# Optimization experiments

Measured on AMD Instinct MI355X. Metric: run time of the kernel, lower is better.

## Reference

```python
import jax, jax.numpy as jnp
import numpy as np

NC = 6            # CPAB tessellation cells (tess_size=6, zero_boundary=True)
DIM = NC - 1      # theta dimension = 5
SIG_LEN = 2048
CHANNELS = 3
BATCH = 256
FC_IN = 64 * 168  # flattened net_part1 output for signal_len=2048
NUM_SCALING = 0   # N in transform_data_ss
EPS_BN = 1e-5


def _cpab_basis():
    """QR null-space basis of the CPAB continuity + zero-boundary constraints.
    Params ordered [a_1,b_1,...,a_NC,b_NC]; v(x)=a_c x + b_c on cell c."""
    nc = NC
    L = np.zeros((nc + 1, 2 * nc))
    for k in range(1, nc):  # continuity at internal knots x_k = k/nc
        xk = k / nc
        L[k - 1, 2 * (k - 1)] = xk
        L[k - 1, 2 * (k - 1) + 1] = 1.0
        L[k - 1, 2 * k] = -xk
        L[k - 1, 2 * k + 1] = -1.0
    L[nc - 1, 1] = 1.0        # v(0) = 0  -> b_1 = 0
    L[nc, 2 * (nc - 1)] = 1.0  # v(1) = 0 -> a_nc + b_nc = 0
    L[nc, 2 * nc - 1] = 1.0
    Q, _ = np.linalg.qr(L.T, mode='complete')
    return np.ascontiguousarray(Q[:, nc + 1:]).astype(np.float32)  # (12, 5)


def _conv1d(x, w, b):
    y = jax.lax.conv_general_dilated(x, w, (1,), 'VALID',
                                     dimension_numbers=('NCH', 'OIH', 'NCH'))
    return y + b[None, :, None]


def _maxpool1d(x, k, s):
    return jax.lax.reduce_window(x, -jnp.inf, jax.lax.max, (1, 1, k), (1, 1, s), 'VALID')


def _bn(x, g, b, m, v):  # eval-mode BatchNorm1d
    return (x - m[None, :, None]) * (g / jnp.sqrt(v + EPS_BN))[None, :, None] + b[None, :, None]


def _integrate(x, A):
    """Exact CPAB 1D flow integration over t=1 with cell-crossing handling.
    x: (B, n) points in [0,1]; A: (B, NC, 2) per-cell (a, b). Monotone
    trajectories cross at most NC-1 boundaries -> fixed NC+1 iterations."""
    a_all, b_all = A[:, :, 0], A[:, :, 1]
    t = jnp.ones_like(x)
    for _ in range(NC + 1):
        c = jnp.clip(jnp.floor(x * NC).astype(jnp.int32), 0, NC - 1)
        a = jnp.take_along_axis(a_all, c, axis=1)
        b = jnp.take_along_axis(b_all, c, axis=1)
        v = a * x + b
        xb = jnp.where(v >= 0, (c + 1).astype(x.dtype) / NC, c.astype(x.dtype) / NC)
        big_a = jnp.abs(a) > 1e-8
        a_s = jnp.where(big_a, a, 1.0)
        z = x + b / a_s        # shifted coord: x(t) = z*exp(a t) - b/a
        zb = xb + b / a_s
        ratio = zb / jnp.where(jnp.abs(z) > 1e-12, z, 1e-12)
        t_exp = jnp.log(jnp.maximum(ratio, 1e-12)) / a_s
        v_s = jnp.where(jnp.abs(v) > 1e-12, v, 1.0)
        t_lin = (xb - x) / v_s
        thit = jnp.where(big_a, t_exp, t_lin)
        valid = (jnp.abs(v) > 1e-12) & (thit > 0) & (jnp.where(big_a, ratio, 1.0) > 0)
        thit = jnp.where(valid, thit, jnp.inf)
        tau = jnp.minimum(t, thit)
        x_new = jnp.where(big_a, z * jnp.exp(a * tau) - (z - x), x + b * tau)
        hit = thit <= t
        nudge = jnp.where(v >= 0, 1e-6, -1e-6)  # push into next cell
        x = jnp.clip(jnp.where(hit, xb + nudge, x_new), 0.0, 1.0)
        t = jnp.maximum(t - tau, 0.0)
    return x


def _interp1d(data, pos):
    """data: (B, L, C); pos: (B, n) in [0,1] -> (B, n, C) linear interpolation."""
    Lw = data.shape[1]
    p = jnp.clip(pos, 0.0, 1.0) * (Lw - 1)
    x0 = jnp.clip(jnp.floor(p).astype(jnp.int32), 0, Lw - 2)
    w = (p - x0.astype(p.dtype))[:, :, None]
    d0 = jnp.take_along_axis(data, x0[:, :, None], axis=1)
    d1 = jnp.take_along_axis(data, (x0 + 1)[:, :, None], axis=1)
    return d0 * (1.0 - w) + d1 * w


def _transform_data_ss(data, theta, basis, outsize, N):
    """CPAB scaling-and-squaring warp of data (B, L, C) by theta (B, DIM)."""
    Bsz = theta.shape[0]
    A = (theta @ basis.T).reshape(Bsz, NC, 2) / (2.0 ** N)
    grid = jnp.linspace(0.0, 1.0, outsize, dtype=data.dtype)
    grid_t = _integrate(jnp.broadcast_to(grid, (Bsz, outsize)), A)
    for _ in range(N):  # squaring: compose the warp with itself
        grid_t = _interp1d(grid_t[:, :, None], grid_t)[:, :, 0]
    return _interp1d(data, grid_t)


def reference(x, conv1_w, conv1_b, bn1_g, bn1_b, bn1_m, bn1_v,
              conv2_w, conv2_b, bn2_g, bn2_b, bn2_m, bn2_v,
              conv3_w, conv3_b, bn3_g, bn3_b, bn3_m, bn3_v,
              fc1_w, fc1_b, fc2_w, fc2_b, fc3_w, fc3_b, fc4_w, fc4_b, basis):
    # localization net (n_recurrence = 1, back_version = True)
    h = jax.nn.relu(_maxpool1d(_bn(_conv1d(x, conv1_w, conv1_b), bn1_g, bn1_b, bn1_m, bn1_v), 3, 2))
    h = jax.nn.relu(_maxpool1d(_bn(_conv1d(h, conv2_w, conv2_b), bn2_g, bn2_b, bn2_m, bn2_v), 3, 3))
    h = jax.nn.relu(_maxpool1d(_bn(_conv1d(h, conv3_w, conv3_b), bn3_g, bn3_b, bn3_m, bn3_v), 3, 2))
    xs = h.reshape(h.shape[0], -1)  # (B, 64*168)
    xs = jax.nn.relu(xs @ fc1_w.T + fc1_b)
    xs = jax.nn.relu(xs @ fc2_w.T + fc2_b)
    xs = jax.nn.relu(xs @ fc3_w.T + fc3_b)
    theta = jnp.tanh(xs @ fc4_w.T + fc4_b)  # (B, 5)
    data = jnp.transpose(x, (0, 2, 1))       # (B, L, C)
    warped = _transform_data_ss(data, theta, basis, SIG_LEN, NUM_SCALING)
    return jnp.transpose(warped, (0, 2, 1))  # (B, C, L)


def setup_inputs() -> dict:
    key = jax.random.key(0)
    ks = jax.random.split(key, 16)
    def nrm(k, shape, scale):
        return (jax.random.normal(k, shape) * scale).astype(jnp.float32)
    inp = {}
    inp['x'] = jax.random.normal(ks[0], (BATCH, CHANNELS, SIG_LEN), dtype=jnp.float32)
    inp['conv1_w'] = nrm(ks[1], (128, CHANNELS, 3), (CHANNELS * 3) ** -0.5)
    inp['conv1_b'] = nrm(ks[2], (128,), 0.01)
    inp['bn1_g'] = jnp.ones((128,), jnp.float32)
    inp['bn1_b'] = jnp.zeros((128,), jnp.float32)
    inp['bn1_m'] = nrm(ks[3], (128,), 0.1)
    inp['bn1_v'] = jnp.ones((128,), jnp.float32)
    inp['conv2_w'] = nrm(ks[4], (64, 128, 5), (128 * 5) ** -0.5)
    inp['conv2_b'] = nrm(ks[5], (64,), 0.01)
    inp['bn2_g'] = jnp.ones((64,), jnp.float32)
    inp['bn2_b'] = jnp.zeros((64,), jnp.float32)
    inp['bn2_m'] = nrm(ks[6], (64,), 0.1)
    inp['bn2_v'] = jnp.ones((64,), jnp.float32)
    inp['conv3_w'] = nrm(ks[7], (64, 64, 3), (64 * 3) ** -0.5)
    inp['conv3_b'] = nrm(ks[8], (64,), 0.01)
    inp['bn3_g'] = jnp.ones((64,), jnp.float32)
    inp['bn3_b'] = jnp.zeros((64,), jnp.float32)
    inp['bn3_m'] = nrm(ks[9], (64,), 0.1)
    inp['bn3_v'] = jnp.ones((64,), jnp.float32)
    inp['fc1_w'] = nrm(ks[10], (48, FC_IN), FC_IN ** -0.5)
    inp['fc1_b'] = jnp.zeros((48,), jnp.float32)
    inp['fc2_w'] = nrm(ks[11], (32, 48), 48 ** -0.5)
    inp['fc2_b'] = jnp.zeros((32,), jnp.float32)
    inp['fc3_w'] = nrm(ks[12], (16, 32), 32 ** -0.5)
    inp['fc3_b'] = jnp.zeros((16,), jnp.float32)
    # near-identity warp head (original zero-inits weight, identity bias)
    inp['fc4_w'] = nrm(ks[13], (DIM, 16), 0.01)
    inp['fc4_b'] = nrm(ks[14], (DIM,), 0.01)
    inp['basis'] = jnp.asarray(_cpab_basis())
    return inp
```

## Files before the change

kernel.cpp:

```cpp
#include <hip/hip_runtime.h>
#include <math.h>

#define BATCH   256
#define SIGLEN  2048
#define L1OUT   1022
#define L2OUT   339
#define L3OUT   168
#define FCIN    10752

#define TP2   21
#define NROW  68
#define H1S   136
#define H1SZ  (NROW*H1S)

#define TU3   28

typedef float f32x4  __attribute__((ext_vector_type(4)));
typedef float f32x16 __attribute__((ext_vector_type(16)));
typedef short s16x8  __attribute__((ext_vector_type(8)));

__device__ __forceinline__ unsigned short f2bf(float f) {
    unsigned int u = __float_as_uint(f);
    return (unsigned short)((u + 0x7fffu + ((u >> 16) & 1u)) >> 16);
}
__device__ __forceinline__ float bf2f(unsigned short h) {
    return __uint_as_float(((unsigned int)h) << 16);
}

__launch_bounds__(256)
__global__ void prep_kernel(
    const float* __restrict__ conv1_b,
    const float* __restrict__ g1, const float* __restrict__ b1,
    const float* __restrict__ m1, const float* __restrict__ v1,
    const float* __restrict__ conv2_w, const float* __restrict__ conv2_b,
    const float* __restrict__ g2, const float* __restrict__ b2,
    const float* __restrict__ m2, const float* __restrict__ v2,
    const float* __restrict__ conv3_w, const float* __restrict__ conv3_b,
    const float* __restrict__ g3, const float* __restrict__ b3,
    const float* __restrict__ m3, const float* __restrict__ v3,
    unsigned short* __restrict__ w2hi, unsigned short* __restrict__ w2lo,
    unsigned short* __restrict__ w3hi, unsigned short* __restrict__ w3lo,
    float* __restrict__ so1, float* __restrict__ so2, float* __restrict__ so3)
{
    int tid = blockIdx.x * 256 + threadIdx.x;
    int stride = gridDim.x * 256;
    for (int i = tid; i < 64*128*5; i += stride) {
        int co = i / 640; int rr = i - co*640; int ci = rr / 5; int k = rr - ci*5;
        float w = conv2_w[i];
        unsigned short hi = f2bf(w);
        unsigned short lo = f2bf(w - bf2f(hi));
        int seg = k*8 + (ci >> 4);
        int dst = ((seg*2 + (co >> 5))*32 + (co & 31))*16 + (ci & 15);
        w2hi[dst] = hi;
        w2lo[dst] = lo;
    }
    for (int i = tid; i < 64*64*3; i += stride) {
        int co = i / 192; int r = i - co*192; int ci = r / 3; int k = r - ci*3;
        float w = conv3_w[i];
        unsigned short hi = f2bf(w);
        unsigned short lo = f2bf(w - bf2f(hi));
        int dst = ((k*2 + (ci >> 5))*64 + co)*32 + (ci & 31);
        w3hi[dst] = hi;
        w3lo[dst] = lo;
    }
    if (tid < 128) {
        float s = g1[tid] / sqrtf(v1[tid] + 1e-5f);
        so1[tid]       = s;
        so1[128 + tid] = (conv1_b[tid] - m1[tid]) * s + b1[tid];
    }
    if (tid < 64) {
        float s2 = g2[tid] / sqrtf(v2[tid] + 1e-5f);
        so2[tid]      = s2;
        so2[64 + tid] = (conv2_b[tid] - m2[tid]) * s2 + b2[tid];
        float s3 = g3[tid] / sqrtf(v3[tid] + 1e-5f);
        so3[tid]      = s3;
        so3[64 + tid] = (conv3_b[tid] - m3[tid]) * s3 + b3[tid];
    }
}

__launch_bounds__(256, 4)
__global__ void conv12_kernel(
    const float* __restrict__ x, const float* __restrict__ w1,
    const unsigned short* __restrict__ w2hi, const unsigned short* __restrict__ w2lo,
    const float* __restrict__ so1, const float* __restrict__ so2,
    unsigned int* __restrict__ h2p)
{
    __shared__ unsigned short h1s[2 * H1SZ];

    int t  = threadIdx.x;
    int b  = blockIdx.x;
    int u0 = blockIdx.y * TP2;
    int q0 = 3 * u0;
    int wv = __builtin_amdgcn_readfirstlane(t >> 6);
    int l  = t & 63;

    float wr[2][9];
    float s1r[2], o1r[2];
    #pragma unroll
    for (int h = 0; h < 2; ++h) {
        int ch = l + 64*h;
        #pragma unroll
        for (int j = 0; j < 9; ++j) wr[h][j] = w1[ch*9 + j];
        s1r[h] = so1[ch]; o1r[h] = so1[128 + ch];
    }
    for (int s = 0; s < 17; ++s) {
        int r = 4*s + wv;
        int xbase = 2*(q0 + r);
        float xv[3][5];
        #pragma unroll
        for (int ci = 0; ci < 3; ++ci) {
            const float* xp = x + (b*3 + ci)*SIGLEN;
            #pragma unroll
            for (int d = 0; d < 5; ++d) {
                int xi = xbase + d; xi = xi < SIGLEN ? xi : SIGLEN - 1;
                xv[ci][d] = xp[xi];
            }
        }
        #pragma unroll
        for (int h = 0; h < 2; ++h) {
            float r0 = 0.f, r1 = 0.f, r2 = 0.f;
            #pragma unroll
            for (int ci = 0; ci < 3; ++ci) {
                float wA = wr[h][ci*3], wB = wr[h][ci*3+1], wC = wr[h][ci*3+2];
                r0 = fmaf(xv[ci][0], wA, fmaf(xv[ci][1], wB, fmaf(xv[ci][2], wC, r0)));
                r1 = fmaf(xv[ci][1], wA, fmaf(xv[ci][2], wB, fmaf(xv[ci][3], wC, r1)));
                r2 = fmaf(xv[ci][2], wA, fmaf(xv[ci][3], wB, fmaf(xv[ci][4], wC, r2)));
            }
            float mx = fmaxf(r0, fmaxf(r1, r2));
            float v  = fmaxf(fmaf(s1r[h], mx, o1r[h]), 0.f);
            unsigned short hi = f2bf(v);
            unsigned short lo = f2bf(v - bf2f(hi));
            h1s[r*H1S + l + 64*h]        = hi;
            h1s[H1SZ + r*H1S + l + 64*h] = lo;
        }
    }
    __syncthreads();

    int chf = wv & 1;
    int kh  = wv >> 1;
    int r32 = l & 31;
    int oct = l >> 5;

    f32x16 acc0 = (f32x16)(0.f);
    f32x16 acc1 = (f32x16)(0.f);
    const unsigned short* whB = w2hi + (chf*32 + r32)*16 + oct*8;
    const unsigned short* wlB = w2lo + (chf*32 + r32)*16 + oct*8;

    #pragma unroll 4
    for (int ss = 0; ss < 20; ++ss) {
        int sg = kh*20 + ss;
        int ks = sg >> 3, cb = sg & 7;
        s16x8 wh = *(const s16x8*)(whB + sg*1024);
        s16x8 wl = *(const s16x8*)(wlB + sg*1024);
        int row0 = r32 + ks;
        int row1 = 32 + r32 + ks;
        s16x8 ah0 = *(const s16x8*)&h1s[row0*H1S + cb*16 + oct*8];
        s16x8 al0 = *(const s16x8*)&h1s[H1SZ + row0*H1S + cb*16 + oct*8];
        s16x8 ah1 = *(const s16x8*)&h1s[row1*H1S + cb*16 + oct*8];
        s16x8 al1 = *(const s16x8*)&h1s[H1SZ + row1*H1S + cb*16 + oct*8];
        acc0 = __builtin_amdgcn_mfma_f32_32x32x16_bf16(ah0, wh, acc0, 0, 0, 0);
        acc1 = __builtin_amdgcn_mfma_f32_32x32x16_bf16(ah1, wh, acc1, 0, 0, 0);
        acc0 = __builtin_amdgcn_mfma_f32_32x32x16_bf16(al0, wh, acc0, 0, 0, 0);
        acc1 = __builtin_amdgcn_mfma_f32_32x32x16_bf16(al1, wh, acc1, 0, 0, 0);
        acc0 = __builtin_amdgcn_mfma_f32_32x32x16_bf16(ah0, wl, acc0, 0, 0, 0);
        acc1 = __builtin_amdgcn_mfma_f32_32x32x16_bf16(ah1, wl, acc1, 0, 0, 0);
    }
    __syncthreads();

    float* c2 = (float*)h1s;
    #pragma unroll
    for (int rg = 0; rg < 16; ++rg) {
        int row = (rg & 3) + 8*(rg >> 2) + 4*oct;
        c2[kh*4160 + row*65        + chf*32 + r32] = acc0[rg];
        c2[kh*4160 + (32 + row)*65 + chf*32 + r32] = acc1[rg];
    }
    __syncthreads();

    #pragma unroll
    for (int it = 0; it < 6; ++it) {
        int idx = t + it*256;
        if (idx < TP2*64) {
            int ul = idx >> 6, co = idx & 63;
            int u = u0 + ul;
            if (u < L2OUT) {
                float v0 = c2[(3*ul  )*65 + co] + c2[4160 + (3*ul  )*65 + co];
                float v1 = c2[(3*ul+1)*65 + co] + c2[4160 + (3*ul+1)*65 + co];
                float v2 = c2[(3*ul+2)*65 + co] + c2[4160 + (3*ul+2)*65 + co];
                float mm = fmaxf(v0, fmaxf(v1, v2));
                float v  = fmaxf(fmaf(so2[co], mm, so2[64 + co]), 0.f);
                unsigned short hi = f2bf(v);
                unsigned short lo = f2bf(v - bf2f(hi));
                h2p[(b*L2OUT + u)*64 + co] = (unsigned int)hi | ((unsigned int)lo << 16);
            }
        }
    }
}

__launch_bounds__(256)
__global__ void tail_kernel(
    const unsigned int* __restrict__ h2p,
    const unsigned short* __restrict__ w3hi, const unsigned short* __restrict__ w3lo,
    const float* __restrict__ so3,
    const float* __restrict__ x,
    const float* __restrict__ fc1_w, const float* __restrict__ fc1_b,
    const float* __restrict__ fc2_w, const float* __restrict__ fc2_b,
    const float* __restrict__ fc3_w, const float* __restrict__ fc3_b,
    const float* __restrict__ fc4_w, const float* __restrict__ fc4_b,
    const float* __restrict__ basis,
    float* __restrict__ out)
{
    __shared__ float xsl[FCIN];
    __shared__ unsigned short h3s[2*66*72];
    __shared__ float c3buf[64*65];
    __shared__ float xs48[48], hl[32], gl[16], thl[5], Al[12];

    int t  = threadIdx.x;
    int b  = blockIdx.x;
    int wv = __builtin_amdgcn_readfirstlane(t >> 6);
    int l  = t & 63;
    int m  = l & 15;
    int qd = l >> 4;

    s16x8 wh[6], wl[6];
    #pragma unroll
    for (int s = 0; s < 6; ++s) {
        wh[s] = *(const s16x8*)(w3hi + s*2048 + (wv*16 + m)*32 + qd*8);
        wl[s] = *(const s16x8*)(w3lo + s*2048 + (wv*16 + m)*32 + qd*8);
    }
    float s3a = so3[t & 63], s3b = so3[64 + (t & 63)];

    for (int ti = 0; ti < 6; ++ti) {
        int u0 = ti * TU3;
        for (int i = t; i < 66*64; i += 256) {
            int r = i >> 6, ci = i & 63;
            int g = 2*u0 + r; g = g > (L2OUT-1) ? (L2OUT-1) : g;
            unsigned int v = h2p[(b*L2OUT + g)*64 + ci];
            h3s[r*72 + ci]          = (unsigned short)(v & 0xffffu);
            h3s[66*72 + r*72 + ci]  = (unsigned short)(v >> 16);
        }
        __syncthreads();

        f32x4 acc[4] = {(f32x4)(0.f), (f32x4)(0.f), (f32x4)(0.f), (f32x4)(0.f)};
        #pragma unroll
        for (int pt = 0; pt < 4; ++pt) {
            #pragma unroll
            for (int s = 0; s < 6; ++s) {
                int row = pt*16 + m + (s >> 1);
                int off = (s & 1)*32 + qd*8;
                s16x8 ah = *(const s16x8*)&h3s[row*72 + off];
                s16x8 al = *(const s16x8*)&h3s[66*72 + row*72 + off];
                acc[pt] = __builtin_amdgcn_mfma_f32_16x16x32_bf16(ah, wh[s], acc[pt], 0, 0, 0);
                acc[pt] = __builtin_amdgcn_mfma_f32_16x16x32_bf16(al, wh[s], acc[pt], 0, 0, 0);
                acc[pt] = __builtin_amdgcn_mfma_f32_16x16x32_bf16(ah, wl[s], acc[pt], 0, 0, 0);
            }
        }
        #pragma unroll
        for (int pt = 0; pt < 4; ++pt)
            #pragma unroll
            for (int rg = 0; rg < 4; ++rg)
                c3buf[(pt*16 + qd*4 + rg)*65 + wv*16 + m] = acc[pt][rg];
        __syncthreads();

        #pragma unroll
        for (int it = 0; it < 7; ++it) {
            int idx = t + it*256;
            if (idx < TU3*64) {
                int co = idx / TU3, ul = idx - co*TU3;
                int p = 2*ul;
                float v0 = c3buf[(p  )*65 + co];
                float v1 = c3buf[(p+1)*65 + co];
                float v2 = c3buf[(p+2)*65 + co];
                float mm = fmaxf(v0, fmaxf(v1, v2));
                xsl[co*L3OUT + u0 + ul] = fmaxf(fmaf(so3[co], mm, so3[64 + co]), 0.f);
            }
        }
        __syncthreads();
    }

    {
        int o0 = wv * 12;
        float acc[12];
        #pragma unroll
        for (int j = 0; j < 12; ++j) acc[j] = 0.f;
        for (int ki = 0; ki < 42; ++ki) {
            int k4 = (ki*64 + l) * 4;
            float4 xv = *(const float4*)&xsl[k4];
            #pragma unroll
            for (int j = 0; j < 12; ++j) {
                float4 wv4 = *(const float4*)&fc1_w[(o0 + j)*FCIN + k4];
                acc[j] = fmaf(xv.x, wv4.x, fmaf(xv.y, wv4.y, fmaf(xv.z, wv4.z, fmaf(xv.w, wv4.w, acc[j]))));
            }
        }
        #pragma unroll
        for (int j = 0; j < 12; ++j) {
            #pragma unroll
            for (int off = 32; off > 0; off >>= 1)
                acc[j] += __shfl_xor(acc[j], off, 64);
        }
        if (l == 0) {
            #pragma unroll
            for (int j = 0; j < 12; ++j)
                xs48[o0 + j] = fmaxf(acc[j] + fc1_b[o0 + j], 0.f);
        }
    }
    __syncthreads();

    if (t < 32) {
        float sv = fc2_b[t];
        #pragma unroll
        for (int k = 0; k < 48; ++k) sv = fmaf(fc2_w[t * 48 + k], xs48[k], sv);
        hl[t] = fmaxf(sv, 0.f);
    }
    __syncthreads();
    if (t < 16) {
        float sv = fc3_b[t];
        #pragma unroll
        for (int k = 0; k < 32; ++k) sv = fmaf(fc3_w[t * 32 + k], hl[k], sv);
        gl[t] = fmaxf(sv, 0.f);
    }
    __syncthreads();
    if (t < 5) {
        float sv = fc4_b[t];
        #pragma unroll
        for (int k = 0; k < 16; ++k) sv = fmaf(fc4_w[t * 16 + k], gl[k], sv);
        thl[t] = tanhf(sv);
    }
    __syncthreads();
    if (t < 12) {
        float sv = 0.f;
        #pragma unroll
        for (int d = 0; d < 5; ++d) sv = fmaf(basis[t * 5 + d], thl[d], sv);
        Al[t] = sv;
    }
    __syncthreads();

    float a_r[6], b_r[6];
    #pragma unroll
    for (int c = 0; c < 6; ++c) { a_r[c] = Al[2*c]; b_r[c] = Al[2*c+1]; }

    for (int ch = 0; ch < 8; ++ch) {
        int i = ch * 256 + t;
        float xp = (float)i / 2047.f;
        float tt = 1.f;
        for (int it = 0; it < 7; ++it) {
            int c = (int)floorf(xp * 6.f);
            c = min(max(c, 0), 5);
            float a  = a_r[c], bb = b_r[c];
            float v  = a * xp + bb;
            float xb = (v >= 0.f) ? (float)(c + 1) / 6.f : (float)c / 6.f;
            bool  big_a = fabsf(a) > 1e-8f;
            float a_s = big_a ? a : 1.f;
            float z   = xp + bb / a_s;
            float zb  = xb + bb / a_s;
            float zden = (fabsf(z) > 1e-12f) ? z : 1e-12f;
            float ratio = zb / zden;
            float t_exp = logf(fmaxf(ratio, 1e-12f)) / a_s;
            float v_s   = (fabsf(v) > 1e-12f) ? v : 1.f;
            float t_lin = (xb - xp) / v_s;
            float thit  = big_a ? t_exp : t_lin;
            bool valid  = (fabsf(v) > 1e-12f) && (thit > 0.f) && ((big_a ? ratio : 1.f) > 0.f);
            if (!valid) thit = __builtin_inff();
            float tau   = fminf(tt, thit);
            float x_new = big_a ? (z * expf(a * tau) - (z - xp)) : (xp + bb * tau);
            bool hit    = (thit <= tt);
            float nudge = (v >= 0.f) ? 1e-6f : -1e-6f;
            xp = hit ? (xb + nudge) : x_new;
            xp = fminf(fmaxf(xp, 0.f), 1.f);
            tt = fmaxf(tt - tau, 0.f);
        }
        float p = fminf(fmaxf(xp, 0.f), 1.f) * 2047.f;
        int i0 = (int)floorf(p);
        i0 = min(max(i0, 0), 2046);
        float w = p - (float)i0;
        #pragma unroll
        for (int c = 0; c < 3; ++c) {
            const float* d = &x[(b * 3 + c) * SIGLEN];
            out[(b * 3 + c) * SIGLEN + i] = d[i0] * (1.f - w) + d[i0 + 1] * w;
        }
    }
    (void)s3a; (void)s3b;
}

extern "C" void kernel_launch(void* const* d_in, const int* in_sizes, int n_in,
                              void* d_out, int out_size, void* d_ws, size_t ws_size,
                              hipStream_t stream) {
    (void)in_sizes; (void)n_in; (void)out_size; (void)ws_size;
    const float* x       = (const float*)d_in[0];
    const float* conv1_w = (const float*)d_in[1];
    const float* conv1_b = (const float*)d_in[2];
    const float* bn1_g   = (const float*)d_in[3];
    const float* bn1_b   = (const float*)d_in[4];
    const float* bn1_m   = (const float*)d_in[5];
    const float* bn1_v   = (const float*)d_in[6];
    const float* conv2_w = (const float*)d_in[7];
    const float* conv2_b = (const float*)d_in[8];
    const float* bn2_g   = (const float*)d_in[9];
    const float* bn2_b   = (const float*)d_in[10];
    const float* bn2_m   = (const float*)d_in[11];
    const float* bn2_v   = (const float*)d_in[12];
    const float* conv3_w = (const float*)d_in[13];
    const float* conv3_b = (const float*)d_in[14];
    const float* bn3_g   = (const float*)d_in[15];
    const float* bn3_b   = (const float*)d_in[16];
    const float* bn3_m   = (const float*)d_in[17];
    const float* bn3_v   = (const float*)d_in[18];
    const float* fc1_w   = (const float*)d_in[19];
    const float* fc1_b   = (const float*)d_in[20];
    const float* fc2_w   = (const float*)d_in[21];
    const float* fc2_b   = (const float*)d_in[22];
    const float* fc3_w   = (const float*)d_in[23];
    const float* fc3_b   = (const float*)d_in[24];
    const float* fc4_w   = (const float*)d_in[25];
    const float* fc4_b   = (const float*)d_in[26];
    const float* basis   = (const float*)d_in[27];

    unsigned short* w2hi = (unsigned short*)d_ws;
    unsigned short* w2lo = w2hi + 40960;
    unsigned short* w3hi = w2lo + 40960;
    unsigned short* w3lo = w3hi + 12288;
    float* ws   = (float*)d_ws;
    float* so1  = ws + 53248;
    float* so2  = so1 + 256;
    float* so3  = so2 + 128;
    unsigned int* h2p = (unsigned int*)(so3 + 128);

    prep_kernel<<<64, 256, 0, stream>>>(
        conv1_b, bn1_g, bn1_b, bn1_m, bn1_v,
        conv2_w, conv2_b, bn2_g, bn2_b, bn2_m, bn2_v,
        conv3_w, conv3_b, bn3_g, bn3_b, bn3_m, bn3_v,
        w2hi, w2lo, w3hi, w3lo, so1, so2, so3);

    dim3 g2(BATCH, (L2OUT + TP2 - 1) / TP2);
    conv12_kernel<<<g2, 256, 0, stream>>>(x, conv1_w, w2hi, w2lo, so1, so2, h2p);

    tail_kernel<<<BATCH, 256, 0, stream>>>(h2p, w3hi, w3lo, so3, x,
                                           fc1_w, fc1_b, fc2_w, fc2_b,
                                           fc3_w, fc3_b, fc4_w, fc4_b, basis,
                                           (float*)d_out);
}
```

Before: 279.6 us.

## Split conv3+fc1 tail across position tiles with partial fc1 sums

```diff
diff --git a/kernel.cpp b/kernel.cpp
--- a/kernel.cpp
+++ b/kernel.cpp
@@ -196,115 +196,126 @@
     }
 }
 
-__launch_bounds__(256)
-__global__ void tail_kernel(
+__launch_bounds__(256, 4)
+__global__ void conv3fc1_kernel(
     const unsigned int* __restrict__ h2p,
     const unsigned short* __restrict__ w3hi, const unsigned short* __restrict__ w3lo,
-    const float* __restrict__ so3,
-    const float* __restrict__ x,
-    const float* __restrict__ fc1_w, const float* __restrict__ fc1_b,
+    const float* __restrict__ so3, const float* __restrict__ fc1_w,
+    float* __restrict__ part)
+{
+    __shared__ unsigned short h3s[2*66*72];
+    __shared__ float c3buf[64*65];
+
+    int t  = threadIdx.x;
+    int b  = blockIdx.x;
+    int ti = blockIdx.y;
+    int u0 = ti * TU3;
+    int wv = __builtin_amdgcn_readfirstlane(t >> 6);
+    int l  = t & 63;
+    int m  = l & 15;
+    int qd = l >> 4;
+
+    for (int i = t; i < 66*64; i += 256) {
+        int r = i >> 6, ci = i & 63;
+        int g = 2*u0 + r; g = g > (L2OUT-1) ? (L2OUT-1) : g;
+        unsigned int v = h2p[(b*L2OUT + g)*64 + ci];
+        h3s[r*72 + ci]         = (unsigned short)(v & 0xffffu);
+        h3s[66*72 + r*72 + ci] = (unsigned short)(v >> 16);
+    }
+    __syncthreads();
+
+    s16x8 wh[6], wl[6];
+    #pragma unroll
+    for (int s = 0; s < 6; ++s) {
+        wh[s] = *(const s16x8*)(w3hi + s*2048 + (wv*16 + m)*32 + qd*8);
+        wl[s] = *(const s16x8*)(w3lo + s*2048 + (wv*16 + m)*32 + qd*8);
+    }
+
+    f32x4 acc[4] = {(f32x4)(0.f), (f32x4)(0.f), (f32x4)(0.f), (f32x4)(0.f)};
+    #pragma unroll
+    for (int pt = 0; pt < 4; ++pt) {
+        #pragma unroll
+        for (int s = 0; s < 6; ++s) {
+            int row = pt*16 + m + (s >> 1);
+            int off = (s & 1)*32 + qd*8;
+            s16x8 ah = *(const s16x8*)&h3s[row*72 + off];
+            s16x8 al = *(const s16x8*)&h3s[66*72 + row*72 + off];
+            acc[pt] = __builtin_amdgcn_mfma_f32_16x16x32_bf16(ah, wh[s], acc[pt], 0, 0, 0);
+            acc[pt] = __builtin_amdgcn_mfma_f32_16x16x32_bf16(al, wh[s], acc[pt], 0, 0, 0);
+            acc[pt] = __builtin_amdgcn_mfma_f32_16x16x32_bf16(ah, wl[s], acc[pt], 0, 0, 0);
+        }
+    }
+    __syncthreads();
+
+    #pragma unroll
+    for (int pt = 0; pt < 4; ++pt)
+        #pragma unroll
+        for (int rg = 0; rg < 4; ++rg)
+            c3buf[(pt*16 + qd*4 + rg)*65 + wv*16 + m] = acc[pt][rg];
+    __syncthreads();
+
+    float s3 = so3[l], o3 = so3[64 + l];
+    float pooled[TU3];
+    #pragma unroll
+    for (int u = 0; u < TU3; ++u) {
+        int p = 2*u;
+        float v0 = c3buf[(p  )*65 + l];
+        float v1 = c3buf[(p+1)*65 + l];
+        float v2 = c3buf[(p+2)*65 + l];
+        pooled[u] = fmaxf(fmaf(s3, fmaxf(v0, fmaxf(v1, v2)), o3), 0.f);
+    }
+
+    int o0 = wv * 12;
+    float fa[12];
+    #pragma unroll
+    for (int j = 0; j < 12; ++j) {
+        const float* wp = fc1_w + (o0 + j)*FCIN + l*L3OUT + u0;
+        float sv = 0.f;
+        #pragma unroll
+        for (int u4 = 0; u4 < TU3; u4 += 4) {
+            float4 w4 = *(const float4*)(wp + u4);
+            sv = fmaf(pooled[u4  ], w4.x, sv);
+            sv = fmaf(pooled[u4+1], w4.y, sv);
+            sv = fmaf(pooled[u4+2], w4.z, sv);
+            sv = fmaf(pooled[u4+3], w4.w, sv);
+        }
+        fa[j] = sv;
+    }
+    #pragma unroll
+    for (int j = 0; j < 12; ++j) {
+        #pragma unroll
+        for (int off = 32; off > 0; off >>= 1)
+            fa[j] += __shfl_xor(fa[j], off, 64);
+    }
+    if (l == 0) {
+        #pragma unroll
+        for (int j = 0; j < 12; ++j)
+            part[(b*6 + ti)*48 + o0 + j] = fa[j];
+    }
+}
+
+__launch_bounds__(256)
+__global__ void warp_kernel(
+    const float* __restrict__ x, const float* __restrict__ part,
+    const float* __restrict__ fc1_b,
     const float* __restrict__ fc2_w, const float* __restrict__ fc2_b,
     const float* __restrict__ fc3_w, const float* __restrict__ fc3_b,
     const float* __restrict__ fc4_w, const float* __restrict__ fc4_b,
     const float* __restrict__ basis,
     float* __restrict__ out)
 {
-    __shared__ float xsl[FCIN];
-    __shared__ unsigned short h3s[2*66*72];
-    __shared__ float c3buf[64*65];
     __shared__ float xs48[48], hl[32], gl[16], thl[5], Al[12];
 
-    int t  = threadIdx.x;
-    int b  = blockIdx.x;
-    int wv = __builtin_amdgcn_readfirstlane(t >> 6);
-    int l  = t & 63;
-    int m  = l & 15;
-    int qd = l >> 4;
-
-    s16x8 wh[6], wl[6];
-    #pragma unroll
-    for (int s = 0; s < 6; ++s) {
-        wh[s] = *(const s16x8*)(w3hi + s*2048 + (wv*16 + m)*32 + qd*8);
-        wl[s] = *(const s16x8*)(w3lo + s*2048 + (wv*16 + m)*32 + qd*8);
-    }
-    float s3a = so3[t & 63], s3b = so3[64 + (t & 63)];
-
-    for (int ti = 0; ti < 6; ++ti) {
-        int u0 = ti * TU3;
-        for (int i = t; i < 66*64; i += 256) {
-            int r = i >> 6, ci = i & 63;
-            int g = 2*u0 + r; g = g > (L2OUT-1) ? (L2OUT-1) : g;
-            unsigned int v = h2p[(b*L2OUT + g)*64 + ci];
-            h3s[r*72 + ci]          = (unsigned short)(v & 0xffffu);
-            h3s[66*72 + r*72 + ci]  = (unsigned short)(v >> 16);
-        }
-        __syncthreads();
-
-        f32x4 acc[4] = {(f32x4)(0.f), (f32x4)(0.f), (f32x4)(0.f), (f32x4)(0.f)};
-        #pragma unroll
-        for (int pt = 0; pt < 4; ++pt) {
-            #pragma unroll
-            for (int s = 0; s < 6; ++s) {
-                int row = pt*16 + m + (s >> 1);
-                int off = (s & 1)*32 + qd*8;
-                s16x8 ah = *(const s16x8*)&h3s[row*72 + off];
-                s16x8 al = *(const s16x8*)&h3s[66*72 + row*72 + off];
-                acc[pt] = __builtin_amdgcn_mfma_f32_16x16x32_bf16(ah, wh[s], acc[pt], 0, 0, 0);
-                acc[pt] = __builtin_amdgcn_mfma_f32_16x16x32_bf16(al, wh[s], acc[pt], 0, 0, 0);
-                acc[pt] = __builtin_amdgcn_mfma_f32_16x16x32_bf16(ah, wl[s], acc[pt], 0, 0, 0);
-            }
-        }
-        #pragma unroll
-        for (int pt = 0; pt < 4; ++pt)
-            #pragma unroll
-            for (int rg = 0; rg < 4; ++rg)
-                c3buf[(pt*16 + qd*4 + rg)*65 + wv*16 + m] = acc[pt][rg];
-        __syncthreads();
-
-        #pragma unroll
-        for (int it = 0; it < 7; ++it) {
-            int idx = t + it*256;
-            if (idx < TU3*64) {
-                int co = idx / TU3, ul = idx - co*TU3;
-                int p = 2*ul;
-                float v0 = c3buf[(p  )*65 + co];
-                float v1 = c3buf[(p+1)*65 + co];
-                float v2 = c3buf[(p+2)*65 + co];
-                float mm = fmaxf(v0, fmaxf(v1, v2));
-                xsl[co*L3OUT + u0 + ul] = fmaxf(fmaf(so3[co], mm, so3[64 + co]), 0.f);
-            }
-        }
-        __syncthreads();
-    }
-
-    {
-        int o0 = wv * 12;
-        float acc[12];
-        #pragma unroll
-        for (int j = 0; j < 12; ++j) acc[j] = 0.f;
-        for (int ki = 0; ki < 42; ++ki) {
-            int k4 = (ki*64 + l) * 4;
-            float4 xv = *(const float4*)&xsl[k4];
-            #pragma unroll
-            for (int j = 0; j < 12; ++j) {
-                float4 wv4 = *(const float4*)&fc1_w[(o0 + j)*FCIN + k4];
-                acc[j] = fmaf(xv.x, wv4.x, fmaf(xv.y, wv4.y, fmaf(xv.z, wv4.z, fmaf(xv.w, wv4.w, acc[j]))));
-            }
-        }
-        #pragma unroll
-        for (int j = 0; j < 12; ++j) {
-            #pragma unroll
-            for (int off = 32; off > 0; off >>= 1)
-                acc[j] += __shfl_xor(acc[j], off, 64);
-        }
-        if (l == 0) {
-            #pragma unroll
-            for (int j = 0; j < 12; ++j)
-                xs48[o0 + j] = fmaxf(acc[j] + fc1_b[o0 + j], 0.f);
-        }
-    }
-    __syncthreads();
-
+    int b = blockIdx.x;
+    int t = threadIdx.x;
+
+    if (t < 48) {
+        float sv = 0.f;
+        #pragma unroll
+        for (int ti = 0; ti < 6; ++ti) sv += part[(b*6 + ti)*48 + t];
+        xs48[t] = fmaxf(sv + fc1_b[t], 0.f);
+    }
+    __syncthreads();
     if (t < 32) {
         float sv = fc2_b[t];
         #pragma unroll
@@ -378,7 +389,6 @@
             out[(b * 3 + c) * SIGLEN + i] = d[i0] * (1.f - w) + d[i0 + 1] * w;
         }
     }
-    (void)s3a; (void)s3b;
 }
 
 extern "C" void kernel_launch(void* const* d_in, const int* in_sizes, int n_in,
@@ -423,6 +433,7 @@
     float* so2  = so1 + 256;
     float* so3  = so2 + 128;
     unsigned int* h2p = (unsigned int*)(so3 + 128);
+    float* part = (float*)(h2p + 5554176);
 
     prep_kernel<<<64, 256, 0, stream>>>(
         conv1_b, bn1_g, bn1_b, bn1_m, bn1_v,
@@ -433,8 +444,10 @@
     dim3 g2(BATCH, (L2OUT + TP2 - 1) / TP2);
     conv12_kernel<<<g2, 256, 0, stream>>>(x, conv1_w, w2hi, w2lo, so1, so2, h2p);
 
-    tail_kernel<<<BATCH, 256, 0, stream>>>(h2p, w3hi, w3lo, so3, x,
-                                           fc1_w, fc1_b, fc2_w, fc2_b,
+    dim3 g3(BATCH, 6);
+    conv3fc1_kernel<<<g3, 256, 0, stream>>>(h2p, w3hi, w3lo, so3, fc1_w, part);
+
+    warp_kernel<<<BATCH, 256, 0, stream>>>(x, part, fc1_b, fc2_w, fc2_b,
                                            fc3_w, fc3_b, fc4_w, fc4_b, basis,
                                            (float*)d_out);
 }
```

After: 362.4 us. 29.6% more time.
